# Kernel optimization log

Measured on AMD Instinct MI355X. Metric: run time of the kernel, lower is better.

Reference implementation:

```python
import jax, jax.numpy as jnp
import numpy as np

D_MODEL = 1024
Q_DIM = K_DIM = V_DIM = 1024
MASKED = True

def setup_inputs() -> dict:
    key = jax.random.key(0)
    ks = jax.random.split(key, 7)
    s = 1.0 / np.sqrt(D_MODEL)
    return {
        "x": jax.random.normal(ks[0], (4, 2048, D_MODEL), dtype=jnp.float32),
        "Wq": jax.random.uniform(ks[1], (D_MODEL, Q_DIM), jnp.float32, -s, s),
        "bq": jax.random.uniform(ks[2], (Q_DIM,), jnp.float32, -s, s),
        "Wk": jax.random.uniform(ks[3], (D_MODEL, K_DIM), jnp.float32, -s, s),
        "bk": jax.random.uniform(ks[4], (K_DIM,), jnp.float32, -s, s),
        "Wv": jax.random.uniform(ks[5], (D_MODEL, V_DIM), jnp.float32, -s, s),
        "bv": jax.random.uniform(ks[6], (V_DIM,), jnp.float32, -s, s),
    }

def reference(x, Wq, bq, Wk, bk, Wv, bv):
    # QKV projections: [b, s, d]
    q = x @ Wq + bq
    k = x @ Wk + bk
    v = x @ Wv + bv
    dk = k.shape[-1]
    # scores: [b, s_q, s_k]
    scores = jnp.einsum('bqd,bkd->bqk', q, k) / jnp.sqrt(jnp.float32(dk))
    if MASKED:
        s = scores.shape[-1]
        tri = jnp.triu(jnp.ones((s, s), dtype=bool), k=1)  # strictly upper
        scores = jnp.where(tri, jnp.float32(-1e9), scores)
    # NOTE: original softmaxes over dim=-2 (the query axis) — faithful here.
    probs = jax.nn.softmax(scores, axis=-2)
    attn = jnp.einsum('bqk,bkd->bqd', probs, v)
    # dropout in eval mode = identity
    return attn
```

## Files before the change

kernel.cpp:

```cpp
#include <hip/hip_runtime.h>

#define DEV __device__ __forceinline__

typedef float f32x4 __attribute__((ext_vector_type(4)));
typedef short short4v __attribute__((ext_vector_type(4)));
typedef short short8v __attribute__((ext_vector_type(8)));
typedef __bf16 bf16x8 __attribute__((ext_vector_type(8)));

#define PSTR  (2048L * 2048)
#define OSTR  (2048L * 1024)

DEV unsigned short f2bf(float f) {
  unsigned int u = __float_as_uint(f);
  u += 0x7fffu + ((u >> 16) & 1u);
  return (unsigned short)(u >> 16);
}
DEV float bf2f(short s) {
  return __uint_as_float(((unsigned int)(unsigned short)s) << 16);
}

DEV void async16(void* lds, const void* g) {
  __builtin_amdgcn_global_load_lds((const __attribute__((address_space(1))) void*)g,
                                   (__attribute__((address_space(3))) void*)lds, 16, 0, 0);
}

DEV float wave_red(float v) {
#pragma unroll
  for (int o = 1; o < 64; o <<= 1) v += __shfl_xor(v, o);
  return v;
}

__global__ void pre_kernel(const float* __restrict__ x, short* __restrict__ xb,
                           const float* __restrict__ Wq, const float* __restrict__ Wk,
                           const float* __restrict__ Wv,
                           short* __restrict__ wqb, short* __restrict__ wkb,
                           short* __restrict__ wvt,
                           const float* __restrict__ bq, const float* __restrict__ bk,
                           float* __restrict__ g, float* __restrict__ h,
                           float* __restrict__ cbuf)
{
  __shared__ float t[32][33];
  const int b = blockIdx.x;
  const int tid = threadIdx.x;
  if (b < 4096) {
    long i = ((long)b * 256 + tid) * 8;
    f32x4 a = *(const f32x4*)(x + i);
    f32x4 c2 = *(const f32x4*)(x + i + 4);
    short8v o;
#pragma unroll
    for (int j = 0; j < 4; ++j) { o[j] = (short)f2bf(a[j]); o[4 + j] = (short)f2bf(c2[j]); }
    *(short8v*)(xb + i) = o;
  } else if (b < 5120) {
    int tb = b - 4096;
    const float* W = (tb < 512) ? Wq : Wk;
    short* Wo = (tb < 512) ? wqb : wkb;
    long i = ((long)(tb & 511) * 256 + tid) * 8;
    f32x4 a = *(const f32x4*)(W + i);
    f32x4 c2 = *(const f32x4*)(W + i + 4);
    short8v o;
#pragma unroll
    for (int j = 0; j < 4; ++j) { o[j] = (short)f2bf(a[j]); o[4 + j] = (short)f2bf(c2[j]); }
    *(short8v*)(Wo + i) = o;
  } else if (b < 6144) {
    int t2 = b - 5120;
    int n0 = (t2 & 31) * 32, k0 = (t2 >> 5) * 32;
    int tx = tid & 31, ty = tid >> 5;
#pragma unroll
    for (int r = 0; r < 32; r += 8) t[ty + r][tx] = Wv[(long)(k0 + ty + r) * 1024 + n0 + tx];
    __syncthreads();
#pragma unroll
    for (int r = 0; r < 32; r += 8)
      wvt[(long)(n0 + ty + r) * 1024 + k0 + tx] = (short)f2bf(t[tx][ty + r]);
  } else if (b < 6656) {
    int local = b - 6144;
    const float* W = (local < 256) ? Wq : Wk;
    const float* bb = (local < 256) ? bk : bq;
    float* out = (local < 256) ? g : h;
    const int d = (local & 255) * 4 + (tid >> 6);
    const int lane = tid & 63;
    const float* row = W + (long)d * 1024 + lane * 16;
    const float* bp = bb + lane * 16;
    float s = 0.f;
#pragma unroll
    for (int q = 0; q < 4; ++q) {
      f32x4 wv = *(const f32x4*)(row + q * 4);
      f32x4 bv2 = *(const f32x4*)(bp + q * 4);
#pragma unroll
      for (int j = 0; j < 4; ++j) s += wv[j] * bv2[j];
    }
    s = wave_red(s);
    if (lane == 0) out[d] = s;
  } else {
    float s = 0.f;
#pragma unroll
    for (int q = 0; q < 4; ++q) s += bq[tid + q * 256] * bk[tid + q * 256];
    s = wave_red(s);
    __shared__ float red[4];
    if ((tid & 63) == 0) red[tid >> 6] = s;
    __syncthreads();
    if (tid == 0) cbuf[0] = red[0] + red[1] + red[2] + red[3];
  }
}

template <typename CT, int MODE>
DEV void gemm_body32(short* As0, short* As1, short* Bs0, short* Bs1,
                     const short* A, const short* Bt, CT* C,
                     int K, int lda, int ldbt, int ldc,
                     const float* bias_m, const float* bias_n, float scale,
                     int bn, int bm)
{
  const int kend = K;

  const int tid = threadIdx.x;
  const int wid = tid >> 6, lane = tid & 63;
  const int wm = wid >> 1, wn = wid & 1;
  const int rC = lane >> 2;
  const int swS = (rC & 3) ^ ((rC >> 2) & 3);
  const int kB = (((lane & 3) ^ swS)) * 8;
  const int fr = lane & 15;
  const int swR = (fr & 3) ^ ((fr >> 2) & 3);
  const int fkB = (((lane >> 4) ^ swR)) * 16;

  const short* Ab = A + (long)bm * 128 * lda + (long)rC * lda + kB;
  const short* Bb = Bt + (long)bn * 128 * ldbt + (long)rC * ldbt + kB;

  f32x4 acc[4][4] = {};

  auto STAGE = [&](short* Asb, short* Bsb, int kk) {
#pragma unroll
    for (int j = 0; j < 2; ++j) {
      int chunk = j * 4 + wid;
      async16(&Asb[chunk * 512], Ab + (long)chunk * 16 * lda + kk);
      async16(&Bsb[chunk * 512], Bb + (long)chunk * 16 * ldbt + kk);
    }
  };

  STAGE(As0, Bs0, 0);
  int cur = 0;
  for (int kk = 0; kk < kend; kk += 32) {
    const short* Ac = cur ? As1 : As0;
    const short* Bc = cur ? Bs1 : Bs0;
    if (kk + 32 < kend) {
      STAGE(cur ? As0 : As1, cur ? Bs0 : Bs1, kk + 32);
      asm volatile("s_waitcnt vmcnt(4)" ::: "memory");
    } else {
      asm volatile("s_waitcnt vmcnt(0)" ::: "memory");
    }
    __builtin_amdgcn_s_barrier();
    __builtin_amdgcn_sched_barrier(0);

    bf16x8 af[4], bf_[4];
#pragma unroll
    for (int i = 0; i < 4; ++i)
      af[i] = *(const bf16x8*)((const char*)Ac + (wm * 64 + i * 16 + fr) * 64 + fkB);
#pragma unroll
    for (int j = 0; j < 4; ++j)
      bf_[j] = *(const bf16x8*)((const char*)Bc + (wn * 64 + j * 16 + fr) * 64 + fkB);
#pragma unroll
    for (int i = 0; i < 4; ++i)
#pragma unroll
      for (int j = 0; j < 4; ++j)
        acc[i][j] = __builtin_amdgcn_mfma_f32_16x16x32_bf16(af[i], bf_[j], acc[i][j], 0, 0, 0);
    __builtin_amdgcn_s_barrier();
    cur ^= 1;
  }

  const int fq = lane >> 4;
  const int rl0 = wm * 64 + fq * 4;
  const int cl0 = wn * 64 + fr;

  short* pt = As0;
#pragma unroll
  for (int i = 0; i < 4; ++i) {
#pragma unroll
    for (int r = 0; r < 4; ++r) {
      int rl = rl0 + i * 16 + r;
      float bmv = bias_m ? bias_m[bm * 128 + rl] : 0.f;
#pragma unroll
      for (int j = 0; j < 4; ++j) {
        int cl = cl0 + j * 16;
        float bnv = bias_n ? bias_n[bn * 128 + cl] : 0.f;
        pt[rl * 128 + cl] = (short)f2bf(acc[i][j][r] * scale + bmv + bnv);
      }
    }
  }
  __syncthreads();
  const long cbase = (long)bm * 128 * ldc + bn * 128;
#pragma unroll
  for (int p2 = 0; p2 < 8; ++p2) {
    int flat = p2 * 2048 + tid * 8;
    int rl = flat >> 7, cl = flat & 127;
    *(short8v*)((short*)C + cbase + (long)rl * ldc + cl) = *(const short8v*)(pt + flat);
  }
}

template <typename CT, int MODE>
DEV void gemm_body64(short* lds,
                     const short* A, const short* Bt, CT* C,
                     int K, int lda, int ldbt, int ldc,
                     float scale,
                     const float* u_vec, const float* w_vec,
                     float* ps_out, int bn, int bm, int bz)
{
  short* As0 = lds;
  short* As1 = lds + 8192;
  short* Bs0 = lds + 16384;
  short* Bs1 = lds + 24576;
  const int kend = (MODE == 2) ? min(K, (bm + 1) * 128) : K;

  const int tid = threadIdx.x;
  const int wid = tid >> 6, lane = tid & 63;
  const int wm = wid >> 1, wn = wid & 1;
  const int lrow = lane >> 3;
  const int lcol = ((lane & 7) ^ lrow) * 8;
  const int fr = lane & 15;
  const int fq = lane >> 4;

  const short* Ab = A + (long)(bm * 128 + lrow) * lda + lcol;
  const short* Bb = Bt + (long)(bn * 128 + lrow) * ldbt + lcol;

  f32x4 acc[4][4] = {};

  auto STAGE = [&](short* Asb, short* Bsb, int kk) {
#pragma unroll
    for (int j = 0; j < 4; ++j) {
      int chunk = j * 4 + wid;
      async16(&Asb[chunk * 512], Ab + (long)chunk * 8 * lda + kk);
      async16(&Bsb[chunk * 512], Bb + (long)chunk * 8 * ldbt + kk);
    }
  };

  STAGE(As0, Bs0, 0);
  int cur = 0;
  for (int kk = 0; kk < kend; kk += 64) {
    const short* Ac = cur ? As1 : As0;
    const short* Bc = cur ? Bs1 : Bs0;
    if (kk + 64 < kend) {
      STAGE(cur ? As0 : As1, cur ? Bs0 : Bs1, kk + 64);
      asm volatile("s_waitcnt vmcnt(8)" ::: "memory");
    } else {
      asm volatile("s_waitcnt vmcnt(0)" ::: "memory");
    }
    __builtin_amdgcn_s_barrier();
    __builtin_amdgcn_sched_barrier(0);

#pragma unroll
    for (int s = 0; s < 2; ++s) {
      bf16x8 af[4], bf_[4];
#pragma unroll
      for (int i = 0; i < 4; ++i) {
        int row = wm * 64 + i * 16 + fr;
        af[i] = *(const bf16x8*)((const char*)Ac + row * 128 +
                                 (((s * 4 + fq) ^ (fr & 7)) * 16));
      }
#pragma unroll
      for (int j = 0; j < 4; ++j) {
        int row = wn * 64 + j * 16 + fr;
        bf_[j] = *(const bf16x8*)((const char*)Bc + row * 128 +
                                  (((s * 4 + fq) ^ (fr & 7)) * 16));
      }
#pragma unroll
      for (int i = 0; i < 4; ++i)
#pragma unroll
        for (int j = 0; j < 4; ++j)
          acc[i][j] = __builtin_amdgcn_mfma_f32_16x16x32_bf16(af[i], bf_[j], acc[i][j], 0, 0, 0);
    }
    __builtin_amdgcn_s_barrier();
    cur ^= 1;
  }

  const int rl0 = wm * 64 + fq * 4;
  const int cl0 = wn * 64 + fr;

  if constexpr (MODE == 2) {
#pragma unroll
    for (int i = 0; i < 4; ++i) {
#pragma unroll
      for (int r = 0; r < 4; ++r) {
        int row = bm * 128 + rl0 + i * 16 + r;
#pragma unroll
        for (int j = 0; j < 4; ++j) {
          int col = bn * 128 + cl0 + j * 16;
          C[(long)row * ldc + col] = acc[i][j][r] * scale;
        }
      }
    }
  } else {
    short* pt = lds;
    if constexpr (MODE == 0) {
#pragma unroll
      for (int i = 0; i < 4; ++i) {
#pragma unroll
        for (int r = 0; r < 4; ++r) {
          int rl = rl0 + i * 16 + r;
#pragma unroll
          for (int j = 0; j < 4; ++j) {
            int cl = cl0 + j * 16;
            pt[rl * 128 + cl] = (short)f2bf(acc[i][j][r] * scale);
          }
        }
      }
    } else {
      float uu[4][4];
#pragma unroll
      for (int i = 0; i < 4; ++i)
#pragma unroll
        for (int r = 0; r < 4; ++r) uu[i][r] = u_vec[bm * 128 + rl0 + i * 16 + r];
#pragma unroll
      for (int j = 0; j < 4; ++j) {
        const int cl = cl0 + j * 16;
        const int col = bn * 128 + cl;
        const float wc = w_vec[col];
#pragma unroll
        for (int i = 0; i < 4; ++i)
#pragma unroll
          for (int r = 0; r < 4; ++r) {
            int rl = rl0 + i * 16 + r;
            int row = bm * 128 + rl;
            float e = (row >= col) ? __expf((acc[i][j][r] + uu[i][r] + wc) * scale) : 0.f;
            pt[rl * 128 + cl] = (short)f2bf(e);
          }
      }
    }
    __syncthreads();
    if constexpr (MODE == 1) {
      if (tid < 128) {
        float s = 0.f;
#pragma unroll 8
        for (int r2 = 0; r2 < 128; ++r2) s += bf2f(pt[r2 * 128 + tid]);
        ps_out[((long)bz * 16 + bm) * 2048 + bn * 128 + tid] = s;
      }
    }
    const long cbase = (long)bm * 128 * ldc + bn * 128;
#pragma unroll
    for (int p2 = 0; p2 < 8; ++p2) {
      int flat = p2 * 2048 + tid * 8;
      int rl = flat >> 7, cl = flat & 127;
      *(short8v*)((short*)C + cbase + (long)rl * ldc + cl) = *(const short8v*)(pt + flat);
    }
  }
}

__global__ __launch_bounds__(256, 2) void pv_gemm(
    const short* __restrict__ A, const short* __restrict__ Bt, float* __restrict__ C,
    long sA, long sBt, long sC)
{
  __shared__ __align__(16) short lds[32768];
  const int k = (int)blockIdx.x;
  const int y = (int)blockIdx.y;
  const int bm = (y < 8) ? (15 - k) : k;
  const int bn = y & 7;
  const int bz = blockIdx.z;
  gemm_body64<float, 2>(lds, A + (long)bz * sA, Bt + (long)bz * sBt, C + (long)bz * sC,
                        2048, 2048, 8192, 1024, 1.f, nullptr, nullptr, nullptr, bn, bm, bz);
}

__global__ __launch_bounds__(256, 4) void aux_kernel(
    const short* __restrict__ wqb, const short* __restrict__ wkb,
    short* __restrict__ Mt,
    const short* __restrict__ xb, const short* __restrict__ wvt,
    const float* __restrict__ bv, short* __restrict__ vt,
    const float* __restrict__ g, const float* __restrict__ h,
    const float* __restrict__ cbuf,
    float* __restrict__ u, float* __restrict__ w)
{
  __shared__ __align__(16) short lds[4][4096];
  int b = (int)blockIdx.x;
  const int k = b & 7;
  const int j = b >> 3;
  if (j < 8) {
    const int id = k * 8 + j;
    gemm_body32<short, 0>(lds[0], lds[1], lds[2], lds[3],
                          wkb, wqb, Mt, 1024, 1024, 1024, 1024,
                          nullptr, nullptr, 1.f, id & 7, id >> 3);
  } else if (j < 72) {
    const int j2 = j - 8;
    const int bn = k * 8 + (j2 & 7);
    const int bm = j2 >> 3;
    gemm_body32<short, 0>(lds[0], lds[1], lds[2], lds[3],
                          wvt, xb, vt, 1024, 1024, 1024, 8192,
                          bv, nullptr, 1.f, bn, bm);
  } else {
    const int id = k * 256 + (j - 72);
    const int wv_ = threadIdx.x >> 6, lane = threadIdx.x & 63;
    const int s = id * 4 + wv_;
    const short* row = xb + (long)s * 1024 + lane * 16;
    const float* gp = g + lane * 16;
    const float* hp = h + lane * 16;
    short8v xa = *(const short8v*)(row);
    short8v xb2 = *(const short8v*)(row + 8);
    float du = 0.f, dw = 0.f;
#pragma unroll
    for (int q = 0; q < 2; ++q) {
      f32x4 ga = *(const f32x4*)(gp + q * 4);
      f32x4 gb = *(const f32x4*)(gp + 8 + q * 4);
      f32x4 ha = *(const f32x4*)(hp + q * 4);
      f32x4 hb = *(const f32x4*)(hp + 8 + q * 4);
#pragma unroll
      for (int i2 = 0; i2 < 4; ++i2) {
        float xv0 = bf2f(xa[q * 4 + i2]);
        float xv1 = bf2f(xb2[q * 4 + i2]);
        du += xv0 * ga[i2] + xv1 * gb[i2];
        dw += xv0 * ha[i2] + xv1 * hb[i2];
      }
    }
    du = wave_red(du);
    dw = wave_red(dw);
    if (lane == 0) { u[s] = du + cbuf[0]; w[s] = dw; }
  }
}

__global__ __launch_bounds__(256, 2) void ygemm(
    const short* __restrict__ xb, const short* __restrict__ Mt,
    short* __restrict__ y)
{
  __shared__ __align__(16) short lds[32768];
  int b = (int)blockIdx.x;
  const int k = b & 7;
  const int j = b >> 3;
  const int bn = j >> 3;
  const int bm = k * 8 + (j & 7);
  gemm_body64<short, 0>(lds, xb, Mt, y, 1024, 1024, 1024, 1024,
                        1.f, nullptr, nullptr, nullptr, bn, bm, 0);
}

__global__ __launch_bounds__(256, 2) void scores_k(
    const short* __restrict__ y, const short* __restrict__ xb,
    short* __restrict__ P, const float* __restrict__ u,
    const float* __restrict__ w, float* __restrict__ psum, int z0)
{
  __shared__ __align__(16) short lds[32768];
  const int nwg = (int)gridDim.x;
  int b = (int)blockIdx.x;
  b = (b & 7) * (nwg >> 3) + (b >> 3);
  const int z = b / 136;
  int idx = b - z * 136;
  int bm = 0;
  while ((bm + 1) * (bm + 2) / 2 <= idx) ++bm;
  int bn = idx - bm * (bm + 1) / 2;
  const long off = (long)(z0 + z) * 2048 * 1024;
  gemm_body64<short, 1>(lds, y + off, xb + off, P + (long)z * PSTR,
                        1024, 1024, 1024, 2048, 0.03125f,
                        u + (long)(z0 + z) * 2048, w + (long)(z0 + z) * 2048,
                        psum, bn, bm, z);
}

__global__ __launch_bounds__(256) void vscale_finv(
    const short* __restrict__ vt, const float* __restrict__ psum,
    short* __restrict__ vts, int b0)
{
  const int z = blockIdx.y;
  const int kc = blockIdx.x;
  const int k0 = kc * 32;
  __shared__ float finv[32];
  const int t = threadIdx.x;
  if (t < 32) {
    const int k = k0 + t;
    float D = 0.f;
    for (int ch = k >> 7; ch < 16; ++ch) D += psum[((long)z * 16 + ch) * 2048 + k];
    finv[t] = 1.f / D;
  }
  __syncthreads();
  const int kg = (t & 3) * 8;
  f32x4 fa = *(const f32x4*)(&finv[kg]);
  f32x4 fb = *(const f32x4*)(&finv[kg + 4]);
  const int dbase = t >> 2;
  const short* src = vt + (long)(b0 + z) * 2048 + k0 + kg;
  short* dst = vts + (long)z * 2048 + k0 + kg;
#pragma unroll 4
  for (int pass = 0; pass < 16; ++pass) {
    const long d = dbase + pass * 64;
    short8v v = *(const short8v*)(src + d * 8192);
    short8v o;
#pragma unroll
    for (int j = 0; j < 4; ++j) {
      o[j]     = (short)f2bf(bf2f(v[j]) * fa[j]);
      o[4 + j] = (short)f2bf(bf2f(v[4 + j]) * fb[j]);
    }
    *(short8v*)(dst + d * 8192) = o;
  }
}

extern "C" void kernel_launch(void* const* d_in, const int* in_sizes, int n_in,
                              void* d_out, int out_size, void* d_ws, size_t ws_size,
                              hipStream_t stream) {
  const float* x  = (const float*)d_in[0];
  const float* Wq = (const float*)d_in[1];
  const float* bq = (const float*)d_in[2];
  const float* Wk = (const float*)d_in[3];
  const float* bk = (const float*)d_in[4];
  const float* Wv = (const float*)d_in[5];
  const float* bv = (const float*)d_in[6];
  float* out = (float*)d_out;

  const size_t SZ_XB  = 8192ull * 1024 * 2;
  const size_t SZ_W   = 1024ull * 1024 * 2;
  const size_t SZ_VT  = 1024ull * 8192 * 2;
  const size_t N_PS   = 4ull * 16 * 2048;
  const size_t SZ_SM  = (N_PS + 8192 * 2 + 1024 * 2 + 64) * 4;
  const size_t SZ_P1  = 2048ull * 2048 * 2;

  char* p = (char*)d_ws;
  short* xb  = (short*)p; p += SZ_XB;
  short* yb  = (short*)p; p += SZ_XB;
  short* wqb = (short*)p; p += SZ_W;
  short* wkb = (short*)p; p += SZ_W;
  short* wvt = (short*)p; p += SZ_W;
  short* Mt  = (short*)p; p += SZ_W;
  short* vt  = (short*)p; p += SZ_VT;
  short* vts = (short*)p; p += SZ_VT;
  float* psum = (float*)p;
  float* u    = psum + N_PS;
  float* w    = u + 8192;
  float* g    = w + 8192;
  float* h    = g + 1024;
  float* cbuf = h + 1024;
  p += SZ_SM;
  size_t fixed = (size_t)(p - (char*)d_ws);
  int nbuf = (ws_size >= fixed + 4 * SZ_P1) ? 4 : 1;
  short* P = (short*)p;

  pre_kernel<<<dim3(6657), dim3(256), 0, stream>>>(
      x, xb, Wq, Wk, Wv, wqb, wkb, wvt, bq, bk, g, h, cbuf);

  aux_kernel<<<dim3(2624), dim3(256), 0, stream>>>(
      wqb, wkb, Mt, xb, wvt, bv, vt, g, h, cbuf, u, w);

  ygemm<<<dim3(512), dim3(256), 0, stream>>>(xb, Mt, yb);

  for (int b0 = 0; b0 < 4; b0 += nbuf) {
    const int nz = nbuf;
    scores_k<<<dim3(136 * nz), dim3(256), 0, stream>>>(
        yb, xb, P, u, w, psum, b0);
    vscale_finv<<<dim3(64, nz), dim3(256), 0, stream>>>(vt, psum, vts, b0);
    pv_gemm<<<dim3(8, 16, nz), dim3(256), 0, stream>>>(
        P, vts, out + (long)b0 * OSTR, PSTR, 2048L, OSTR);
  }
}
```

Before: 150.5 us.

## Move Mt and V GEMMs to 64-wide K tiles and fuse u/w into y-GEMM

```diff
diff --git a/kernel.cpp b/kernel.cpp
--- a/kernel.cpp
+++ b/kernel.cpp
@@ -103,102 +103,10 @@
 }
 
 template <typename CT, int MODE>
-DEV void gemm_body32(short* As0, short* As1, short* Bs0, short* Bs1,
-                     const short* A, const short* Bt, CT* C,
-                     int K, int lda, int ldbt, int ldc,
-                     const float* bias_m, const float* bias_n, float scale,
-                     int bn, int bm)
-{
-  const int kend = K;
-
-  const int tid = threadIdx.x;
-  const int wid = tid >> 6, lane = tid & 63;
-  const int wm = wid >> 1, wn = wid & 1;
-  const int rC = lane >> 2;
-  const int swS = (rC & 3) ^ ((rC >> 2) & 3);
-  const int kB = (((lane & 3) ^ swS)) * 8;
-  const int fr = lane & 15;
-  const int swR = (fr & 3) ^ ((fr >> 2) & 3);
-  const int fkB = (((lane >> 4) ^ swR)) * 16;
-
-  const short* Ab = A + (long)bm * 128 * lda + (long)rC * lda + kB;
-  const short* Bb = Bt + (long)bn * 128 * ldbt + (long)rC * ldbt + kB;
-
-  f32x4 acc[4][4] = {};
-
-  auto STAGE = [&](short* Asb, short* Bsb, int kk) {
-#pragma unroll
-    for (int j = 0; j < 2; ++j) {
-      int chunk = j * 4 + wid;
-      async16(&Asb[chunk * 512], Ab + (long)chunk * 16 * lda + kk);
-      async16(&Bsb[chunk * 512], Bb + (long)chunk * 16 * ldbt + kk);
-    }
-  };
-
-  STAGE(As0, Bs0, 0);
-  int cur = 0;
-  for (int kk = 0; kk < kend; kk += 32) {
-    const short* Ac = cur ? As1 : As0;
-    const short* Bc = cur ? Bs1 : Bs0;
-    if (kk + 32 < kend) {
-      STAGE(cur ? As0 : As1, cur ? Bs0 : Bs1, kk + 32);
-      asm volatile("s_waitcnt vmcnt(4)" ::: "memory");
-    } else {
-      asm volatile("s_waitcnt vmcnt(0)" ::: "memory");
-    }
-    __builtin_amdgcn_s_barrier();
-    __builtin_amdgcn_sched_barrier(0);
-
-    bf16x8 af[4], bf_[4];
-#pragma unroll
-    for (int i = 0; i < 4; ++i)
-      af[i] = *(const bf16x8*)((const char*)Ac + (wm * 64 + i * 16 + fr) * 64 + fkB);
-#pragma unroll
-    for (int j = 0; j < 4; ++j)
-      bf_[j] = *(const bf16x8*)((const char*)Bc + (wn * 64 + j * 16 + fr) * 64 + fkB);
-#pragma unroll
-    for (int i = 0; i < 4; ++i)
-#pragma unroll
-      for (int j = 0; j < 4; ++j)
-        acc[i][j] = __builtin_amdgcn_mfma_f32_16x16x32_bf16(af[i], bf_[j], acc[i][j], 0, 0, 0);
-    __builtin_amdgcn_s_barrier();
-    cur ^= 1;
-  }
-
-  const int fq = lane >> 4;
-  const int rl0 = wm * 64 + fq * 4;
-  const int cl0 = wn * 64 + fr;
-
-  short* pt = As0;
-#pragma unroll
-  for (int i = 0; i < 4; ++i) {
-#pragma unroll
-    for (int r = 0; r < 4; ++r) {
-      int rl = rl0 + i * 16 + r;
-      float bmv = bias_m ? bias_m[bm * 128 + rl] : 0.f;
-#pragma unroll
-      for (int j = 0; j < 4; ++j) {
-        int cl = cl0 + j * 16;
-        float bnv = bias_n ? bias_n[bn * 128 + cl] : 0.f;
-        pt[rl * 128 + cl] = (short)f2bf(acc[i][j][r] * scale + bmv + bnv);
-      }
-    }
-  }
-  __syncthreads();
-  const long cbase = (long)bm * 128 * ldc + bn * 128;
-#pragma unroll
-  for (int p2 = 0; p2 < 8; ++p2) {
-    int flat = p2 * 2048 + tid * 8;
-    int rl = flat >> 7, cl = flat & 127;
-    *(short8v*)((short*)C + cbase + (long)rl * ldc + cl) = *(const short8v*)(pt + flat);
-  }
-}
-
-template <typename CT, int MODE>
 DEV void gemm_body64(short* lds,
                      const short* A, const short* Bt, CT* C,
                      int K, int lda, int ldbt, int ldc,
-                     float scale,
+                     float scale, const float* bias_m,
                      const float* u_vec, const float* w_vec,
                      float* ps_out, int bn, int bm, int bz)
 {
@@ -293,10 +201,11 @@
 #pragma unroll
         for (int r = 0; r < 4; ++r) {
           int rl = rl0 + i * 16 + r;
+          float bmv = bias_m ? bias_m[bm * 128 + rl] : 0.f;
 #pragma unroll
           for (int j = 0; j < 4; ++j) {
             int cl = cl0 + j * 16;
-            pt[rl * 128 + cl] = (short)f2bf(acc[i][j][r] * scale);
+            pt[rl * 128 + cl] = (short)f2bf(acc[i][j][r] * scale + bmv);
           }
         }
       }
@@ -341,47 +250,46 @@
   }
 }
 
-__global__ __launch_bounds__(256, 2) void pv_gemm(
-    const short* __restrict__ A, const short* __restrict__ Bt, float* __restrict__ C,
-    long sA, long sBt, long sC)
-{
-  __shared__ __align__(16) short lds[32768];
-  const int k = (int)blockIdx.x;
-  const int y = (int)blockIdx.y;
-  const int bm = (y < 8) ? (15 - k) : k;
-  const int bn = y & 7;
-  const int bz = blockIdx.z;
-  gemm_body64<float, 2>(lds, A + (long)bz * sA, Bt + (long)bz * sBt, C + (long)bz * sC,
-                        2048, 2048, 8192, 1024, 1.f, nullptr, nullptr, nullptr, bn, bm, bz);
-}
-
-__global__ __launch_bounds__(256, 4) void aux_kernel(
+__global__ __launch_bounds__(256, 2) void aux64(
     const short* __restrict__ wqb, const short* __restrict__ wkb,
     short* __restrict__ Mt,
     const short* __restrict__ xb, const short* __restrict__ wvt,
-    const float* __restrict__ bv, short* __restrict__ vt,
+    const float* __restrict__ bv, short* __restrict__ vt)
+{
+  __shared__ __align__(16) short lds[32768];
+  int b = (int)blockIdx.x;
+  const int k = b & 7;
+  const int j = b >> 3;
+  if (j < 64) {
+    const int bn = k * 8 + (j & 7);
+    const int bm = j >> 3;
+    gemm_body64<short, 0>(lds, wvt, xb, vt, 1024, 1024, 1024, 8192,
+                          1.f, bv, nullptr, nullptr, nullptr, bn, bm, 0);
+  } else {
+    const int id = k * 8 + (j - 64);
+    gemm_body64<short, 0>(lds, wkb, wqb, Mt, 1024, 1024, 1024, 1024,
+                          1.f, nullptr, nullptr, nullptr, nullptr, id & 7, id >> 3, 0);
+  }
+}
+
+__global__ __launch_bounds__(256, 2) void yuw(
+    const short* __restrict__ xb, const short* __restrict__ Mt,
+    short* __restrict__ y,
     const float* __restrict__ g, const float* __restrict__ h,
     const float* __restrict__ cbuf,
     float* __restrict__ u, float* __restrict__ w)
 {
-  __shared__ __align__(16) short lds[4][4096];
+  __shared__ __align__(16) short lds[32768];
   int b = (int)blockIdx.x;
   const int k = b & 7;
   const int j = b >> 3;
-  if (j < 8) {
-    const int id = k * 8 + j;
-    gemm_body32<short, 0>(lds[0], lds[1], lds[2], lds[3],
-                          wkb, wqb, Mt, 1024, 1024, 1024, 1024,
-                          nullptr, nullptr, 1.f, id & 7, id >> 3);
-  } else if (j < 72) {
-    const int j2 = j - 8;
-    const int bn = k * 8 + (j2 & 7);
-    const int bm = j2 >> 3;
-    gemm_body32<short, 0>(lds[0], lds[1], lds[2], lds[3],
-                          wvt, xb, vt, 1024, 1024, 1024, 8192,
-                          bv, nullptr, 1.f, bn, bm);
+  if (j < 64) {
+    const int bn = j >> 3;
+    const int bm = k * 8 + (j & 7);
+    gemm_body64<short, 0>(lds, xb, Mt, y, 1024, 1024, 1024, 1024,
+                          1.f, nullptr, nullptr, nullptr, nullptr, bn, bm, 0);
   } else {
-    const int id = k * 256 + (j - 72);
+    const int id = k * 256 + (j - 64);
     const int wv_ = threadIdx.x >> 6, lane = threadIdx.x & 63;
     const int s = id * 4 + wv_;
     const short* row = xb + (long)s * 1024 + lane * 16;
@@ -408,20 +316,6 @@
     dw = wave_red(dw);
     if (lane == 0) { u[s] = du + cbuf[0]; w[s] = dw; }
   }
-}
-
-__global__ __launch_bounds__(256, 2) void ygemm(
-    const short* __restrict__ xb, const short* __restrict__ Mt,
-    short* __restrict__ y)
-{
-  __shared__ __align__(16) short lds[32768];
-  int b = (int)blockIdx.x;
-  const int k = b & 7;
-  const int j = b >> 3;
-  const int bn = j >> 3;
-  const int bm = k * 8 + (j & 7);
-  gemm_body64<short, 0>(lds, xb, Mt, y, 1024, 1024, 1024, 1024,
-                        1.f, nullptr, nullptr, nullptr, bn, bm, 0);
 }
 
 __global__ __launch_bounds__(256, 2) void scores_k(
@@ -440,9 +334,24 @@
   int bn = idx - bm * (bm + 1) / 2;
   const long off = (long)(z0 + z) * 2048 * 1024;
   gemm_body64<short, 1>(lds, y + off, xb + off, P + (long)z * PSTR,
-                        1024, 1024, 1024, 2048, 0.03125f,
+                        1024, 1024, 1024, 2048, 0.03125f, nullptr,
                         u + (long)(z0 + z) * 2048, w + (long)(z0 + z) * 2048,
                         psum, bn, bm, z);
+}
+
+__global__ __launch_bounds__(256, 2) void pv_gemm(
+    const short* __restrict__ A, const short* __restrict__ Bt, float* __restrict__ C,
+    long sA, long sBt, long sC)
+{
+  __shared__ __align__(16) short lds[32768];
+  const int k = (int)blockIdx.x;
+  const int y = (int)blockIdx.y;
+  const int bm = (y < 8) ? (15 - k) : k;
+  const int bn = y & 7;
+  const int bz = blockIdx.z;
+  gemm_body64<float, 2>(lds, A + (long)bz * sA, Bt + (long)bz * sBt, C + (long)bz * sC,
+                        2048, 2048, 8192, 1024, 1.f, nullptr, nullptr, nullptr,
+                        nullptr, bn, bm, bz);
 }
 
 __global__ __launch_bounds__(256) void vscale_finv(
@@ -523,10 +432,9 @@
   pre_kernel<<<dim3(6657), dim3(256), 0, stream>>>(
       x, xb, Wq, Wk, Wv, wqb, wkb, wvt, bq, bk, g, h, cbuf);
 
-  aux_kernel<<<dim3(2624), dim3(256), 0, stream>>>(
-      wqb, wkb, Mt, xb, wvt, bv, vt, g, h, cbuf, u, w);
-
-  ygemm<<<dim3(512), dim3(256), 0, stream>>>(xb, Mt, yb);
+  aux64<<<dim3(576), dim3(256), 0, stream>>>(wqb, wkb, Mt, xb, wvt, bv, vt);
+
+  yuw<<<dim3(2560), dim3(256), 0, stream>>>(xb, Mt, yb, g, h, cbuf, u, w);
 
   for (int b0 = 0; b0 < 4; b0 += nbuf) {
     const int nz = nbuf;
```

After: 150.6 us. No clear change (+0.1%).
